# Optimization experiments

Measured on AMD Instinct MI355X. Metric: run time of the kernel, lower is better.

Reference implementation:

```python
import jax, jax.numpy as jnp
import numpy as np

B, T, W, N, D, H, E, NB = 1, 2048, 15, 512, 1024, 150, 20, 10
CP = 2  # coref_prop iterations
NEG = 1e23


def _bucket(d):
    # Lee-et-al style distance bucketing into NB=10 buckets
    d = jnp.clip(d, 0, None)
    logd = (jnp.floor(jnp.log(jnp.maximum(d.astype(jnp.float32), 1.0)) / np.log(2.0)).astype(jnp.int32) + 3)
    return jnp.clip(jnp.where(d <= 4, d, logd), 0, NB - 1)


def _pairs(u, begin, end, Wl, bl, Wr, br, Wp, bp, Edist, Wd, bd, W1, b1, Wo, bo):
    # OptFFpairs: left + right + prod*prod + dist-embedding -> 2-layer FF -> scalar
    l = u @ Wl + bl                                   # [B,N,H]
    r = u @ Wr + br
    s = u @ Wp + bp
    dist = _bucket(begin[:, :, None] - end[:, None, :])  # [B,N,N]
    pe = Edist[dist] @ Wd + bd                        # [B,N,N,H]
    h = l[:, :, None, :] + r[:, None, :, :] + s[:, :, None, :] * s[:, None, :, :] + pe
    h = jax.nn.relu(h)
    h = jax.nn.relu(h @ W1 + b1)
    return (h @ Wo + bo)[..., 0]                      # [B,N,N]


def _add_scores(cs, ss):
    # coref_add_scores: add unary span scores symmetrically, zero the diagonal
    s = cs + ss + jnp.swapaxes(ss, -1, -2)            # ss: [B,N,1]
    eye = jnp.eye(s.shape[-1], dtype=s.dtype)
    return s * (1.0 - eye)


def _overwrite_spans(all_vecs, idx, lengths, values):
    b, t, w, d = all_vecs.shape
    flat = all_vecs.reshape(b, t * w, d)
    k = idx.shape[1]
    mask = (jnp.arange(k)[None, :] < lengths[:, None])[..., None]   # [B,K,1]
    bidx = jnp.arange(b)[:, None]
    orig = flat[bidx, idx]                                          # [B,K,D]
    flat = flat.at[bidx, idx].set(jnp.where(mask, values, orig))
    return flat.reshape(b, t, w, d)


def setup_inputs() -> dict:
    key = jax.random.key(0)
    ks = jax.random.split(key, 24)
    sc = 0.02
    inp = {
        'all_span_vecs': jax.random.normal(ks[0], (B, T, W, D), jnp.float32),
        'span_vecs': jax.random.normal(ks[1], (B, N, D), jnp.float32),
        'span_scores': jax.random.normal(ks[2], (B, N, 1), jnp.float32),
        'triangular_mask': jnp.tril(jnp.ones((N, N), jnp.float32))[None].repeat(B, 0),
        'span_begin': jnp.sort(jax.random.randint(ks[3], (B, N), 0, T), axis=-1).astype(jnp.int32),
        'span_end': jax.random.randint(ks[4], (B, N), 0, T).astype(jnp.int32),
        'prune_indices': jnp.sort(jax.random.permutation(ks[5], T * W)[:N])[None].astype(jnp.int64),
        'span_lengths': jnp.full((B,), N, jnp.int32),
        # OptFFpairs params
        'Wl': jax.random.normal(ks[6], (D, H)) * sc, 'bl': jnp.zeros((H,)),
        'Wr': jax.random.normal(ks[7], (D, H)) * sc, 'br': jnp.zeros((H,)),
        'Wp': jax.random.normal(ks[8], (D, H)) * sc, 'bp': jnp.zeros((H,)),
        'Edist': jax.random.normal(ks[9], (NB, E)) * sc,
        'Wd': jax.random.normal(ks[10], (E, H)) * sc, 'bd': jnp.zeros((H,)),
        'W1': jax.random.normal(ks[11], (H, H)) * sc, 'b1': jnp.zeros((H,)),
        'Wo': jax.random.normal(ks[12], (H, 1)) * sc, 'bo': jnp.zeros((1,)),
        # MyGate params
        'Wg': jax.random.normal(ks[13], (2 * D, D)) * sc, 'bg': jnp.zeros((D,)),
        # coref_pruner params
        'Wpr': jax.random.normal(ks[14], (D, 1)) * sc, 'bpr': jnp.zeros((1,)),
    }
    return inp


def reference(all_span_vecs, span_vecs, span_scores, triangular_mask,
              Wl, bl, Wr, br, Wp, bp, Edist, Wd, bd, W1, b1, Wo, bo,
              Wg, bg, Wpr, bpr,
              span_begin, span_end, prune_indices, span_lengths):
    pargs = (Wl, bl, Wr, br, Wp, bp, Edist, Wd, bd, W1, b1, Wo, bo)
    update = span_vecs
    scores = _pairs(update, span_begin, span_end, *pargs)
    scores = _add_scores(scores, span_scores)
    for _ in range(CP):
        probs = jax.nn.softmax(scores - (1.0 - triangular_mask) * NEG, axis=-1)
        ctxt = jnp.einsum('bij,bjd->bid', probs, update)
        g = jax.nn.sigmoid(jnp.concatenate([update, ctxt], axis=-1) @ Wg + bg)
        update = g * update + (1.0 - g) * ctxt
        scores = _pairs(update, span_begin, span_end, *pargs)
        scores = _add_scores(scores, update @ Wpr + bpr)
    all_out = _overwrite_spans(all_span_vecs, prune_indices, span_lengths, update)
    return (all_out, update, scores)
```

## Files before the change

kernel.cpp:

```cpp
#include <hip/hip_runtime.h>
#include <hip/hip_bf16.h>
#include <cstdint>
#include <cstddef>

typedef __attribute__((ext_vector_type(8))) short short8;
typedef __attribute__((ext_vector_type(4))) float floatx4;

#define MFMA_BF16(a,b,c) __builtin_amdgcn_mfma_f32_16x16x32_bf16((a),(b),(c),0,0,0)

__device__ __forceinline__ float bf2f(short s) {
    return __uint_as_float(((unsigned int)(unsigned short)s) << 16);
}
__device__ __forceinline__ unsigned short f2bf(float f) {
    unsigned int u = __float_as_uint(f);
    u += 0x7FFFu + ((u >> 16) & 1u);
    return (unsigned short)(u >> 16);
}
__device__ __forceinline__ int bucketd(int d) {
    if (d < 0) d = 0;
    if (d <= 4) return d;
    int b = 34 - __clz(d);
    return b > 9 ? 9 : b;
}

__global__ __launch_bounds__(256) void k_prep(
    const float* __restrict__ Wg, const float* __restrict__ Wl, const float* __restrict__ Wr,
    const float* __restrict__ Wp, const float* __restrict__ Wpr,
    const float* __restrict__ span_vecs, const float* __restrict__ span_scores,
    const float* __restrict__ W1g, const float* __restrict__ Edist,
    const float* __restrict__ Wd, const float* __restrict__ bd,
    const float* __restrict__ b1, const float* __restrict__ Wo,
    const float* __restrict__ bl, const float* __restrict__ br, const float* __restrict__ bp,
    const float* __restrict__ bpr,
    unsigned short* __restrict__ WgT, unsigned short* __restrict__ WprojT,
    unsigned short* __restrict__ updT, unsigned short* __restrict__ ubf0,
    float* __restrict__ updatef, float* __restrict__ ss0,
    unsigned short* __restrict__ W1T, unsigned short* __restrict__ Pb,
    float* __restrict__ b1p, float* __restrict__ wop, float* __restrict__ bproj)
{
    __shared__ float tile[32][33];
    int b = blockIdx.x, tid = threadIdx.x;
    if (b < 3040) {
        const float* in; unsigned short* out; int R, C, ldo, rb, cb;
        if (b < 2048)      { in = Wg; out = WgT; R = 2048; C = 1024; ldo = 2048; rb = (b & 63) * 32; cb = (b >> 6) * 32; }
        else if (b < 2208) { int t = b - 2048; in = Wl; out = WprojT;            R = 1024; C = 150; ldo = 1024; rb = (t & 31) * 32; cb = (t >> 5) * 32; }
        else if (b < 2368) { int t = b - 2208; in = Wr; out = WprojT + 192*1024; R = 1024; C = 150; ldo = 1024; rb = (t & 31) * 32; cb = (t >> 5) * 32; }
        else if (b < 2528) { int t = b - 2368; in = Wp; out = WprojT + 384*1024; R = 1024; C = 150; ldo = 1024; rb = (t & 31) * 32; cb = (t >> 5) * 32; }
        else               { int t = b - 2528; in = span_vecs; out = updT;       R = 512;  C = 1024; ldo = 512;  rb = (t & 15) * 32; cb = (t >> 4) * 32; }
        int tx = tid & 31, ty = tid >> 5;
#pragma unroll
        for (int k = 0; k < 4; ++k) {
            int r = rb + ty + k*8, c = cb + tx;
            if (r < R && c < C) tile[ty + k*8][tx] = in[(size_t)r*C + c];
        }
        __syncthreads();
#pragma unroll
        for (int k = 0; k < 4; ++k) {
            int c = cb + ty + k*8, r = rb + tx;
            if (r < R && c < C) out[(size_t)c*ldo + r] = f2bf(tile[tx][ty + k*8]);
        }
        return;
    }
    int g = (b - 3040) * 256 + tid;
    const int gsz = 512 * 256;
    for (int i = g; i < 512*1024; i += gsz) {
        float v = span_vecs[i];
        updatef[i] = v;
        ubf0[(i >> 10)*2048 + (i & 1023)] = f2bf(v);
    }
    for (int i = g; i < 512; i += gsz) ss0[i] = span_scores[i];
    for (int i = g; i < 160*168; i += gsz) {
        int n = i / 168, k = i % 168;
        W1T[i] = f2bf((n < 150 && k < 150) ? W1g[k*150 + n] : 0.f);
    }
    for (int i = g; i < 10*168; i += gsz) {
        int bk = i / 168, h = i % 168;
        float v = 0.f;
        if (h < 150) {
            v = bd[h];
            for (int e = 0; e < 20; ++e) v += Edist[bk*20 + e] * Wd[e*150 + h];
        }
        Pb[i] = f2bf(v);
    }
    for (int i = g; i < 160; i += gsz) {
        b1p[i] = (i < 150) ? b1[i] : 0.f;
        wop[i] = (i < 150) ? Wo[i] : 0.f;
    }
    for (int i = g; i < 640; i += gsz) {
        float v = 0.f;
        if (i < 150) v = bl[i];
        else if (i >= 192 && i < 342) v = br[i - 192];
        else if (i >= 384 && i < 534) v = bp[i - 384];
        else if (i == 576) v = bpr[0];
        bproj[i] = v;
    }
    for (int i = g; i < 42*1024; i += gsz) { WprojT[150*1024 + i] = 0; WprojT[342*1024 + i] = 0; WprojT[534*1024 + i] = 0; }
    for (int i = g; i < 1024; i += gsz) WprojT[576*1024 + i] = f2bf(Wpr[i]);
    for (int i = g; i < 63*1024; i += gsz) WprojT[577*1024 + i] = 0;
}

__global__ __launch_bounds__(256, 4) void k_gemm(
    const unsigned short* __restrict__ A, int lda,
    const unsigned short* __restrict__ BT, int ldb,
    int K, const float* __restrict__ bias,
    float* __restrict__ Cf,
    unsigned short* __restrict__ Cb, int ldcb,
    const float* __restrict__ uf, const float* __restrict__ cf,
    float* __restrict__ uout, unsigned short* __restrict__ updTout,
    float* __restrict__ ss1, int mode)
{
    __shared__ __align__(16) unsigned short As[32*72];
    __shared__ __align__(16) unsigned short Bs[64*72];
    int tid = threadIdx.x;
    int lane = tid & 63, w = tid >> 6;
    int wy = w >> 1, wx = w & 1;
    int ln15 = lane & 15, kg = lane >> 4;
    int m0 = blockIdx.x * 32, n0 = blockIdx.y * 64;
    int rA = tid >> 3, c8 = (tid & 7) * 8;
    const unsigned short* pA  = A  + (size_t)(m0 + rA)*lda + c8;
    const unsigned short* pB0 = BT + (size_t)(n0 + rA)*ldb + c8;
    const unsigned short* pB1 = pB0 + (size_t)32*ldb;
    int nk = K >> 6;
    uint4 ra[2], rb0[2], rb1[2];
    ra[0]  = *(const uint4*)pA;        ra[1]  = *(const uint4*)(pA + 64);
    rb0[0] = *(const uint4*)pB0;       rb0[1] = *(const uint4*)(pB0 + 64);
    rb1[0] = *(const uint4*)pB1;       rb1[1] = *(const uint4*)(pB1 + 64);
    floatx4 acc[2] = {};
    for (int k = 0; k < nk; ++k) {
        int cur = k & 1;
        __syncthreads();
        *(uint4*)(&As[rA*72 + c8])        = ra[cur];
        *(uint4*)(&Bs[rA*72 + c8])        = rb0[cur];
        *(uint4*)(&Bs[(rA + 32)*72 + c8]) = rb1[cur];
        int kn = (k + 2) << 6;
        if (kn < K) {
            ra[cur]  = *(const uint4*)(pA + kn);
            rb0[cur] = *(const uint4*)(pB0 + kn);
            rb1[cur] = *(const uint4*)(pB1 + kn);
        }
        __syncthreads();
#pragma unroll
        for (int ks = 0; ks < 2; ++ks) {
            int ko = ks*32 + kg*8;
            short8 a  = *(const short8*)(&As[(wy*16 + ln15)*72 + ko]);
            short8 b0 = *(const short8*)(&Bs[(wx*32 + ln15)*72 + ko]);
            short8 b1 = *(const short8*)(&Bs[(wx*32 + 16 + ln15)*72 + ko]);
            acc[0] = MFMA_BF16(a, b0, acc[0]);
            acc[1] = MFMA_BF16(a, b1, acc[1]);
        }
    }
#pragma unroll
    for (int nt = 0; nt < 2; ++nt) {
        int n  = n0 + wx*32 + nt*16 + ln15;
        int mb = m0 + wy*16 + kg*4;
        if (mode == 0) {
            float b_ = bias[n];
#pragma unroll
            for (int rg = 0; rg < 4; ++rg) {
                float v = acc[nt][rg] + b_;
                Cb[(size_t)(mb + rg)*ldcb + n] = f2bf(v);
                if (n == 576) ss1[mb + rg] = v;
            }
        } else if (mode == 1) {
#pragma unroll
            for (int rg = 0; rg < 4; ++rg) {
                float v = acc[nt][rg];
                Cf[(size_t)(mb + rg)*1024 + n] = v;
                Cb[(size_t)(mb + rg)*ldcb + n] = f2bf(v);
            }
        } else {
            float b_ = bias[n];
            ushort4 tv; unsigned short* tvp = &tv.x;
#pragma unroll
            for (int rg = 0; rg < 4; ++rg) {
                float v = acc[nt][rg] + b_;
                float gg = 1.f / (1.f + __expf(-v));
                size_t off = (size_t)(mb + rg)*1024 + n;
                float nu = gg*uf[off] + (1.f - gg)*cf[off];
                uout[off] = nu;
                unsigned short nb = f2bf(nu);
                Cb[(size_t)(mb + rg)*ldcb + n] = nb;
                tvp[rg] = nb;
            }
            *(ushort4*)(updTout + (size_t)n*512 + mb) = tv;
        }
    }
}

__global__ __launch_bounds__(256) void k_softmax(const float* __restrict__ scores,
                                                 unsigned short* __restrict__ probsb)
{
    int i = blockIdx.x;
    int tid = threadIdx.x;
    int lane = tid & 63, w = tid >> 6;
    __shared__ float red[8];
    int j0 = tid, j1 = tid + 256;
    bool v0 = (j0 <= i), v1 = (j1 <= i);
    float x0 = v0 ? scores[(size_t)i*512 + j0] : -1e30f;
    float x1 = v1 ? scores[(size_t)i*512 + j1] : -1e30f;
    float mx = fmaxf(x0, x1);
    for (int off = 32; off; off >>= 1) mx = fmaxf(mx, __shfl_xor(mx, off));
    if (lane == 0) red[w] = mx;
    __syncthreads();
    mx = fmaxf(fmaxf(red[0], red[1]), fmaxf(red[2], red[3]));
    float p0 = v0 ? __expf(x0 - mx) : 0.f;
    float p1 = v1 ? __expf(x1 - mx) : 0.f;
    float sm = p0 + p1;
    for (int off = 32; off; off >>= 1) sm += __shfl_xor(sm, off);
    if (lane == 0) red[4 + w] = sm;
    __syncthreads();
    float inv = 1.f / (red[4] + red[5] + red[6] + red[7]);
    probsb[(size_t)i*512 + j0] = f2bf(p0 * inv);
    probsb[(size_t)i*512 + j1] = f2bf(p1 * inv);
}

__global__ __launch_bounds__(512, 2) void k_pair(
    const unsigned short* __restrict__ lrsb,
    const unsigned short* __restrict__ Pb,
    const unsigned short* __restrict__ W1Tg,
    const float* __restrict__ b1p, const float* __restrict__ wop,
    const float* __restrict__ bo,
    const float* __restrict__ ssbuf,
    const int* __restrict__ beginp, const int* __restrict__ endp,
    float* __restrict__ scoresOut)
{
    __shared__ __align__(16) unsigned short smR[74*168];
    __shared__ __align__(16) unsigned short smB[2][160*36];
    int tid = threadIdx.x;
    int i0 = blockIdx.x * 16, j0 = blockIdx.y * 16;
    for (int c = tid; c < 74*21; c += 512) {
        int row = c / 21, c8 = (c % 21) * 8;
        const unsigned short* src;
        if (row < 16)      src = lrsb + (size_t)(i0 + row)*640 + c8;
        else if (row < 32) src = lrsb + (size_t)(i0 + row - 16)*640 + 384 + c8;
        else if (row < 48) src = lrsb + (size_t)(j0 + row - 32)*640 + 192 + c8;
        else if (row < 64) src = lrsb + (size_t)(j0 + row - 48)*640 + 384 + c8;
        else               src = Pb + (size_t)(row - 64)*168 + c8;
        *(uint4*)(&smR[row*168 + c8]) = *(const uint4*)src;
    }
    int lane = tid & 63, w = tid >> 6;
    int ln15 = lane & 15, kg = lane >> 4;
    int iw = i0 + 2*w;
    int ej = endp[j0 + ln15];
    int da = bucketd(beginp[iw] - ej);
    int db = bucketd(beginp[iw + 1] - ej);
    int rW = tid >> 2, cW = (tid & 3) * 8;
    int rW2 = 128 + rW;
    bool has2 = (tid < 128);
    uint4 w0 = *(const uint4*)(W1Tg + (size_t)rW*168 + cW);
    uint4 w1 = has2 ? *(const uint4*)(W1Tg + (size_t)rW2*168 + cW) : make_uint4(0,0,0,0);
    floatx4 acc[2][10] = {};
    for (int kb = 0; kb < 5; ++kb) {
        int cur = kb & 1;
        *(uint4*)(&smB[cur][rW*36 + cW]) = w0;
        if (has2) *(uint4*)(&smB[cur][rW2*36 + cW]) = w1;
        if (kb < 4) {
            int kf = (kb + 1)*32;
            w0 = *(const uint4*)(W1Tg + (size_t)rW*168 + kf + cW);
            if (has2) w1 = *(const uint4*)(W1Tg + (size_t)rW2*168 + kf + cW);
        }
        __syncthreads();
        int ko = kb*32 + kg*8;
        short8 rv  = *(const short8*)(&smR[(32 + ln15)*168 + ko]);
        short8 sjv = *(const short8*)(&smR[(48 + ln15)*168 + ko]);
        short8 hf[2];
#pragma unroll
        for (int mt = 0; mt < 2; ++mt) {
            int ri = 2*w + mt;
            short8 lv  = *(const short8*)(&smR[ri*168 + ko]);
            short8 siv = *(const short8*)(&smR[(16 + ri)*168 + ko]);
            int d = mt ? db : da;
            short8 pv  = *(const short8*)(&smR[(64 + d)*168 + ko]);
#pragma unroll
            for (int t = 0; t < 8; ++t) {
                float h = bf2f(lv[t]) + bf2f(rv[t]) + bf2f(siv[t]) * bf2f(sjv[t]) + bf2f(pv[t]);
                h = fmaxf(h, 0.f);
                hf[mt][t] = (short)f2bf(h);
            }
        }
#pragma unroll
        for (int nt = 0; nt < 10; ++nt) {
            short8 bv = *(const short8*)(&smB[cur][(nt*16 + ln15)*36 + kg*8]);
            acc[0][nt] = MFMA_BF16(hf[0], bv, acc[0][nt]);
            acc[1][nt] = MFMA_BF16(hf[1], bv, acc[1][nt]);
        }
    }
    float part[2][4] = {};
#pragma unroll
    for (int nt = 0; nt < 10; ++nt) {
        int n = nt*16 + ln15;
        float b1v = b1p[n], wv = wop[n];
#pragma unroll
        for (int mt = 0; mt < 2; ++mt)
#pragma unroll
            for (int rg = 0; rg < 4; ++rg)
                part[mt][rg] += fmaxf(acc[mt][nt][rg] + b1v, 0.f) * wv;
    }
    float bo0 = bo[0];
#pragma unroll
    for (int mt = 0; mt < 2; ++mt) {
#pragma unroll
        for (int rg = 0; rg < 4; ++rg) {
            float p = part[mt][rg];
            p += __shfl_xor(p, 1); p += __shfl_xor(p, 2);
            p += __shfl_xor(p, 4); p += __shfl_xor(p, 8);
            part[mt][rg] = p;
        }
        if (ln15 == 0) {
            int i = iw + mt;
            float ssi = ssbuf[i];
            int jb = j0 + kg*4;
            float r0 = part[mt][0] + bo0 + ssi + ssbuf[jb + 0]; if (i == jb + 0) r0 = 0.f;
            float r1 = part[mt][1] + bo0 + ssi + ssbuf[jb + 1]; if (i == jb + 1) r1 = 0.f;
            float r2 = part[mt][2] + bo0 + ssi + ssbuf[jb + 2]; if (i == jb + 2) r2 = 0.f;
            float r3 = part[mt][3] + bo0 + ssi + ssbuf[jb + 3]; if (i == jb + 3) r3 = 0.f;
            float4 vv; vv.x = r0; vv.y = r1; vv.z = r2; vv.w = r3;
            *(float4*)(scoresOut + (size_t)i*512 + jb) = vv;
        }
    }
}

__global__ __launch_bounds__(256) void k_final(const float* __restrict__ allv,
                                               const int* __restrict__ prune,
                                               const int* __restrict__ lengths,
                                               const float* __restrict__ updatef,
                                               float* __restrict__ out)
{
    int row = blockIdx.x;
    if (row < 30720) {
        int len = lengths[0];
        if (len > 512) len = 512;
        int lo = 0, hi = len;
        while (lo < hi) { int mid = (lo + hi) >> 1; if (prune[mid] < row) lo = mid + 1; else hi = mid; }
        bool found = (lo < len) && (prune[lo] == row);
        const float4* src = found ? (const float4*)(updatef + (size_t)lo*1024)
                                  : (const float4*)(allv + (size_t)row*1024);
        ((float4*)(out + (size_t)row*1024))[threadIdx.x] = src[threadIdx.x];
    } else {
        int k = row - 30720;
        ((float4*)(out + (size_t)row*1024))[threadIdx.x] =
            ((const float4*)(updatef + (size_t)k*1024))[threadIdx.x];
    }
}

extern "C" void kernel_launch(void* const* d_in, const int* in_sizes, int n_in,
                              void* d_out, int out_size, void* d_ws, size_t ws_size,
                              hipStream_t stream) {
    const float* all_span    = (const float*)d_in[0];
    const float* span_vecs   = (const float*)d_in[1];
    const float* span_scores = (const float*)d_in[2];
    const int*   beginp      = (const int*)d_in[4];
    const int*   endp        = (const int*)d_in[5];
    const int*   prune       = (const int*)d_in[6];
    const int*   lengths     = (const int*)d_in[7];
    const float* Wl = (const float*)d_in[8];  const float* bl = (const float*)d_in[9];
    const float* Wr = (const float*)d_in[10]; const float* br = (const float*)d_in[11];
    const float* Wp = (const float*)d_in[12]; const float* bp = (const float*)d_in[13];
    const float* Edist = (const float*)d_in[14];
    const float* Wd = (const float*)d_in[15]; const float* bd = (const float*)d_in[16];
    const float* W1 = (const float*)d_in[17]; const float* b1 = (const float*)d_in[18];
    const float* Wo = (const float*)d_in[19]; const float* bo = (const float*)d_in[20];
    const float* Wg = (const float*)d_in[21]; const float* bg = (const float*)d_in[22];
    const float* Wpr = (const float*)d_in[23]; const float* bpr = (const float*)d_in[24];

    char* wsb = (char*)d_ws;
    size_t o = 0;
    auto nxt = [&](size_t b) { size_t r = o; o += (b + 255) & ~(size_t)255; return r; };
    float* updatef  = (float*)(wsb + nxt(512*1024*4));
    float* ctxtf    = (float*)(wsb + nxt(512*1024*4));
    float* scoresws = (float*)(wsb + nxt(512*512*4));
    float* ss0      = (float*)(wsb + nxt(512*4));
    float* ss1      = (float*)(wsb + nxt(512*4));
    float* bproj    = (float*)(wsb + nxt(640*4));
    float* b1p      = (float*)(wsb + nxt(160*4));
    float* wop      = (float*)(wsb + nxt(160*4));
    unsigned short* ubf0    = (unsigned short*)(wsb + nxt(512*2048*2));
    unsigned short* ubf1    = (unsigned short*)(wsb + nxt(512*2048*2));
    unsigned short* updT    = (unsigned short*)(wsb + nxt(1024*512*2));
    unsigned short* probsb  = (unsigned short*)(wsb + nxt(512*512*2));
    unsigned short* lrsb    = (unsigned short*)(wsb + nxt(512*640*2));
    unsigned short* WgT     = (unsigned short*)(wsb + nxt(1024*2048*2));
    unsigned short* WprojT  = (unsigned short*)(wsb + nxt(640*1024*2));
    unsigned short* W1T     = (unsigned short*)(wsb + nxt(160*168*2));
    unsigned short* Pb      = (unsigned short*)(wsb + nxt(10*168*2));

    float* outp = (float*)d_out;
    float* out_scores = outp + 31457280 + 524288;

    k_prep<<<3552, 256, 0, stream>>>(Wg, Wl, Wr, Wp, Wpr, span_vecs, span_scores,
                                     W1, Edist, Wd, bd, b1, Wo, bl, br, bp, bpr,
                                     WgT, WprojT, updT, ubf0, updatef, ss0,
                                     W1T, Pb, b1p, wop, bproj);

    k_gemm<<<dim3(16, 10), 256, 0, stream>>>(ubf0, 2048, WprojT, 1024, 1024, bproj,
                                             nullptr, lrsb, 640,
                                             nullptr, nullptr, nullptr, nullptr, ss1, 0);
    k_pair<<<dim3(32, 32), 512, 0, stream>>>(lrsb, Pb, W1T, b1p, wop, bo, ss0, beginp, endp, scoresws);

    unsigned short* ucur = ubf0;
    unsigned short* unxt = ubf1;
    for (int it = 0; it < 2; ++it) {
        k_softmax<<<512, 256, 0, stream>>>(scoresws, probsb);
        k_gemm<<<dim3(16, 16), 256, 0, stream>>>(probsb, 512, updT, 512, 512, nullptr,
                                                 ctxtf, ucur + 1024, 2048,
                                                 nullptr, nullptr, nullptr, nullptr, nullptr, 1);
        k_gemm<<<dim3(16, 16), 256, 0, stream>>>(ucur, 2048, WgT, 2048, 2048, bg,
                                                 nullptr, unxt, 2048,
                                                 updatef, ctxtf, updatef, updT, nullptr, 2);
        k_gemm<<<dim3(16, 10), 256, 0, stream>>>(unxt, 2048, WprojT, 1024, 1024, bproj,
                                                 nullptr, lrsb, 640,
                                                 nullptr, nullptr, nullptr, nullptr, ss1, 0);
        float* sdst = (it == 1) ? out_scores : scoresws;
        k_pair<<<dim3(32, 32), 512, 0, stream>>>(lrsb, Pb, W1T, b1p, wop, bo, ss1, beginp, endp, sdst);
        unsigned short* t = ucur; ucur = unxt; unxt = t;
    }

    k_final<<<31232, 256, 0, stream>>>(all_span, prune, lengths, updatef, outp);
}
```

Baseline: 536.6 us.

## Fuse all stages into one persistent kernel with software grid barriers

Replaces the sequence of prep, GEMM, pair, softmax and final-copy launches with a single persistent kernel of 256 blocks of 512 threads. A counter-based global barrier separates the phases, and each phase loops over its tiles or rows by block index. The GEMM tile grows to 64x64 so the 8 waves per block are used. This removes per-launch overhead and idle gaps between launches. In exchange, the memory-bound prep and final-copy phases run at low occupancy, many blocks sit idle in the small GEMM phases, and each barrier adds spin-wait latency.

```diff
diff --git a/kernel.cpp b/kernel.cpp
--- a/kernel.cpp
+++ b/kernel.cpp
@@ -7,6 +7,7 @@
 typedef __attribute__((ext_vector_type(4))) float floatx4;
 
 #define MFMA_BF16(a,b,c) __builtin_amdgcn_mfma_f32_16x16x32_bf16((a),(b),(c),0,0,0)
+#define NBLK 256
 
 __device__ __forceinline__ float bf2f(short s) {
     return __uint_as_float(((unsigned int)(unsigned short)s) << 16);
@@ -23,7 +24,23 @@
     return b > 9 ? 9 : b;
 }
 
-__global__ __launch_bounds__(256) void k_prep(
+__device__ __forceinline__ void gbar(unsigned* cnt, int idx) {
+    __syncthreads();
+    if (threadIdx.x == 0) {
+        __threadfence();
+        __hip_atomic_fetch_add(&cnt[idx], 1u, __ATOMIC_RELAXED, __HIP_MEMORY_SCOPE_AGENT);
+        while (__hip_atomic_load(&cnt[idx], __ATOMIC_RELAXED, __HIP_MEMORY_SCOPE_AGENT) < (unsigned)NBLK)
+            __builtin_amdgcn_s_sleep(8);
+        __threadfence();
+    }
+    __syncthreads();
+}
+
+__global__ void k_zero(unsigned* __restrict__ cnt) {
+    if (threadIdx.x < 64) cnt[threadIdx.x] = 0;
+}
+
+__device__ void prep_phase(char* smc, int tid,
     const float* __restrict__ Wg, const float* __restrict__ Wl, const float* __restrict__ Wr,
     const float* __restrict__ Wp, const float* __restrict__ Wpr,
     const float* __restrict__ span_vecs, const float* __restrict__ span_scores,
@@ -38,31 +55,40 @@
     unsigned short* __restrict__ W1T, unsigned short* __restrict__ Pb,
     float* __restrict__ b1p, float* __restrict__ wop, float* __restrict__ bproj)
 {
-    __shared__ float tile[32][33];
-    int b = blockIdx.x, tid = threadIdx.x;
-    if (b < 3040) {
-        const float* in; unsigned short* out; int R, C, ldo, rb, cb;
-        if (b < 2048)      { in = Wg; out = WgT; R = 2048; C = 1024; ldo = 2048; rb = (b & 63) * 32; cb = (b >> 6) * 32; }
-        else if (b < 2208) { int t = b - 2048; in = Wl; out = WprojT;            R = 1024; C = 150; ldo = 1024; rb = (t & 31) * 32; cb = (t >> 5) * 32; }
-        else if (b < 2368) { int t = b - 2208; in = Wr; out = WprojT + 192*1024; R = 1024; C = 150; ldo = 1024; rb = (t & 31) * 32; cb = (t >> 5) * 32; }
-        else if (b < 2528) { int t = b - 2368; in = Wp; out = WprojT + 384*1024; R = 1024; C = 150; ldo = 1024; rb = (t & 31) * 32; cb = (t >> 5) * 32; }
-        else               { int t = b - 2528; in = span_vecs; out = updT;       R = 512;  C = 1024; ldo = 512;  rb = (t & 15) * 32; cb = (t >> 4) * 32; }
-        int tx = tid & 31, ty = tid >> 5;
-#pragma unroll
-        for (int k = 0; k < 4; ++k) {
-            int r = rb + ty + k*8, c = cb + tx;
-            if (r < R && c < C) tile[ty + k*8][tx] = in[(size_t)r*C + c];
-        }
-        __syncthreads();
-#pragma unroll
-        for (int k = 0; k < 4; ++k) {
-            int c = cb + ty + k*8, r = rb + tx;
-            if (r < R && c < C) out[(size_t)c*ldo + r] = f2bf(tile[tx][ty + k*8]);
-        }
-        return;
-    }
-    int g = (b - 3040) * 256 + tid;
-    const int gsz = 512 * 256;
+    float (*tp)[32][33] = (float (*)[32][33])smc;
+    int half = tid >> 8, t256 = tid & 255;
+    int tx = t256 & 31, ty = t256 >> 5;
+    for (int it = 0; it < 6; ++it) {
+        int t = it*512 + blockIdx.x*2 + half;
+        const float* in = nullptr; unsigned short* out = nullptr;
+        int R = 0, C = 0, ldo = 0, rb = 0, cb = 0;
+        bool act = (t < 3040);
+        if (act) {
+            if (t < 2048)      { in = Wg; out = WgT; R = 2048; C = 1024; ldo = 2048; rb = (t & 63)*32; cb = (t >> 6)*32; }
+            else if (t < 2208) { int q = t - 2048; in = Wl; out = WprojT;            R = 1024; C = 150; ldo = 1024; rb = (q & 31)*32; cb = (q >> 5)*32; }
+            else if (t < 2368) { int q = t - 2208; in = Wr; out = WprojT + 192*1024; R = 1024; C = 150; ldo = 1024; rb = (q & 31)*32; cb = (q >> 5)*32; }
+            else if (t < 2528) { int q = t - 2368; in = Wp; out = WprojT + 384*1024; R = 1024; C = 150; ldo = 1024; rb = (q & 31)*32; cb = (q >> 5)*32; }
+            else               { int q = t - 2528; in = span_vecs; out = updT;       R = 512;  C = 1024; ldo = 512;  rb = (q & 15)*32; cb = (q >> 4)*32; }
+        }
+        if (act) {
+#pragma unroll
+            for (int k = 0; k < 4; ++k) {
+                int r = rb + ty + k*8, c = cb + tx;
+                if (r < R && c < C) tp[half][ty + k*8][tx] = in[(size_t)r*C + c];
+            }
+        }
+        __syncthreads();
+        if (act) {
+#pragma unroll
+            for (int k = 0; k < 4; ++k) {
+                int c = cb + ty + k*8, r = rb + tx;
+                if (r < R && c < C) out[(size_t)c*ldo + r] = f2bf(tp[half][tx][ty + k*8]);
+            }
+        }
+        __syncthreads();
+    }
+    int g = blockIdx.x*512 + tid;
+    const int gsz = NBLK*512;
     for (int i = g; i < 512*1024; i += gsz) {
         float v = span_vecs[i];
         updatef[i] = v;
@@ -99,44 +125,40 @@
     for (int i = g; i < 63*1024; i += gsz) WprojT[577*1024 + i] = 0;
 }
 
-__global__ __launch_bounds__(256, 4) void k_gemm(
+__device__ void gemm_phase(char* smc, int tid,
     const unsigned short* __restrict__ A, int lda,
     const unsigned short* __restrict__ BT, int ldb,
-    int K, const float* __restrict__ bias,
-    float* __restrict__ Cf,
-    unsigned short* __restrict__ Cb, int ldcb,
+    int K, int mtiles, int ntiles, const float* __restrict__ bias,
+    float* __restrict__ Cf, unsigned short* __restrict__ Cb, int ldcb,
     const float* __restrict__ uf, const float* __restrict__ cf,
     float* __restrict__ uout, unsigned short* __restrict__ updTout,
     float* __restrict__ ss1, int mode)
 {
-    __shared__ __align__(16) unsigned short As[32*72];
-    __shared__ __align__(16) unsigned short Bs[64*72];
-    int tid = threadIdx.x;
+    int b = blockIdx.x;
+    if (b >= mtiles*ntiles) return;
+    unsigned short* As = (unsigned short*)smc;
+    unsigned short* Bs = (unsigned short*)(smc + 64*72*2);
+    int m0 = (b % mtiles)*64, n0 = (b / mtiles)*64;
     int lane = tid & 63, w = tid >> 6;
     int wy = w >> 1, wx = w & 1;
     int ln15 = lane & 15, kg = lane >> 4;
-    int m0 = blockIdx.x * 32, n0 = blockIdx.y * 64;
-    int rA = tid >> 3, c8 = (tid & 7) * 8;
-    const unsigned short* pA  = A  + (size_t)(m0 + rA)*lda + c8;
-    const unsigned short* pB0 = BT + (size_t)(n0 + rA)*ldb + c8;
-    const unsigned short* pB1 = pB0 + (size_t)32*ldb;
+    int rA = tid >> 3, c8 = (tid & 7)*8;
+    const unsigned short* pA = A  + (size_t)(m0 + rA)*lda + c8;
+    const unsigned short* pB = BT + (size_t)(n0 + rA)*ldb + c8;
+    uint4 ra[2], rb[2];
+    ra[0] = *(const uint4*)pA;        rb[0] = *(const uint4*)pB;
+    ra[1] = *(const uint4*)(pA + 64); rb[1] = *(const uint4*)(pB + 64);
+    floatx4 acc[2] = {};
     int nk = K >> 6;
-    uint4 ra[2], rb0[2], rb1[2];
-    ra[0]  = *(const uint4*)pA;        ra[1]  = *(const uint4*)(pA + 64);
-    rb0[0] = *(const uint4*)pB0;       rb0[1] = *(const uint4*)(pB0 + 64);
-    rb1[0] = *(const uint4*)pB1;       rb1[1] = *(const uint4*)(pB1 + 64);
-    floatx4 acc[2] = {};
     for (int k = 0; k < nk; ++k) {
         int cur = k & 1;
         __syncthreads();
-        *(uint4*)(&As[rA*72 + c8])        = ra[cur];
-        *(uint4*)(&Bs[rA*72 + c8])        = rb0[cur];
-        *(uint4*)(&Bs[(rA + 32)*72 + c8]) = rb1[cur];
+        *(uint4*)(&As[rA*72 + c8]) = ra[cur];
+        *(uint4*)(&Bs[rA*72 + c8]) = rb[cur];
         int kn = (k + 2) << 6;
         if (kn < K) {
-            ra[cur]  = *(const uint4*)(pA + kn);
-            rb0[cur] = *(const uint4*)(pB0 + kn);
-            rb1[cur] = *(const uint4*)(pB1 + kn);
+            ra[cur] = *(const uint4*)(pA + kn);
+            rb[cur] = *(const uint4*)(pB + kn);
         }
         __syncthreads();
 #pragma unroll
@@ -187,160 +209,212 @@
     }
 }
 
-__global__ __launch_bounds__(256) void k_softmax(const float* __restrict__ scores,
-                                                 unsigned short* __restrict__ probsb)
-{
-    int i = blockIdx.x;
-    int tid = threadIdx.x;
+__device__ void softmax_phase(char* smc, int tid,
+    const float* __restrict__ scores, unsigned short* __restrict__ probsb)
+{
+    float* red = (float*)smc;
     int lane = tid & 63, w = tid >> 6;
-    __shared__ float red[8];
-    int j0 = tid, j1 = tid + 256;
-    bool v0 = (j0 <= i), v1 = (j1 <= i);
-    float x0 = v0 ? scores[(size_t)i*512 + j0] : -1e30f;
-    float x1 = v1 ? scores[(size_t)i*512 + j1] : -1e30f;
-    float mx = fmaxf(x0, x1);
-    for (int off = 32; off; off >>= 1) mx = fmaxf(mx, __shfl_xor(mx, off));
-    if (lane == 0) red[w] = mx;
-    __syncthreads();
-    mx = fmaxf(fmaxf(red[0], red[1]), fmaxf(red[2], red[3]));
-    float p0 = v0 ? __expf(x0 - mx) : 0.f;
-    float p1 = v1 ? __expf(x1 - mx) : 0.f;
-    float sm = p0 + p1;
-    for (int off = 32; off; off >>= 1) sm += __shfl_xor(sm, off);
-    if (lane == 0) red[4 + w] = sm;
-    __syncthreads();
-    float inv = 1.f / (red[4] + red[5] + red[6] + red[7]);
-    probsb[(size_t)i*512 + j0] = f2bf(p0 * inv);
-    probsb[(size_t)i*512 + j1] = f2bf(p1 * inv);
-}
-
-__global__ __launch_bounds__(512, 2) void k_pair(
-    const unsigned short* __restrict__ lrsb,
-    const unsigned short* __restrict__ Pb,
+    for (int r = blockIdx.x; r < 512; r += NBLK) {
+        bool v = (tid <= r);
+        float x = v ? scores[(size_t)r*512 + tid] : -1e30f;
+        float mx = x;
+        for (int off = 32; off; off >>= 1) mx = fmaxf(mx, __shfl_xor(mx, off));
+        if (lane == 0) red[w] = mx;
+        __syncthreads();
+        mx = red[0];
+#pragma unroll
+        for (int q = 1; q < 8; ++q) mx = fmaxf(mx, red[q]);
+        float p = v ? __expf(x - mx) : 0.f;
+        float s = p;
+        for (int off = 32; off; off >>= 1) s += __shfl_xor(s, off);
+        __syncthreads();
+        if (lane == 0) red[w] = s;
+        __syncthreads();
+        float tot = red[0];
+#pragma unroll
+        for (int q = 1; q < 8; ++q) tot += red[q];
+        probsb[(size_t)r*512 + tid] = f2bf(p / tot);
+        __syncthreads();
+    }
+}
+
+__device__ void pair_phase(char* smc, int tid,
+    const unsigned short* __restrict__ lrsb, const unsigned short* __restrict__ Pb,
     const unsigned short* __restrict__ W1Tg,
-    const float* __restrict__ b1p, const float* __restrict__ wop,
-    const float* __restrict__ bo,
+    const float* __restrict__ b1p, const float* __restrict__ wop, const float* __restrict__ bo,
     const float* __restrict__ ssbuf,
     const int* __restrict__ beginp, const int* __restrict__ endp,
     float* __restrict__ scoresOut)
 {
-    __shared__ __align__(16) unsigned short smR[74*168];
-    __shared__ __align__(16) unsigned short smB[2][160*36];
-    int tid = threadIdx.x;
-    int i0 = blockIdx.x * 16, j0 = blockIdx.y * 16;
-    for (int c = tid; c < 74*21; c += 512) {
-        int row = c / 21, c8 = (c % 21) * 8;
-        const unsigned short* src;
-        if (row < 16)      src = lrsb + (size_t)(i0 + row)*640 + c8;
-        else if (row < 32) src = lrsb + (size_t)(i0 + row - 16)*640 + 384 + c8;
-        else if (row < 48) src = lrsb + (size_t)(j0 + row - 32)*640 + 192 + c8;
-        else if (row < 64) src = lrsb + (size_t)(j0 + row - 48)*640 + 384 + c8;
-        else               src = Pb + (size_t)(row - 64)*168 + c8;
-        *(uint4*)(&smR[row*168 + c8]) = *(const uint4*)src;
-    }
+    unsigned short* smR = (unsigned short*)smc;
+    unsigned short* smB = (unsigned short*)(smc + 74*168*2);
     int lane = tid & 63, w = tid >> 6;
     int ln15 = lane & 15, kg = lane >> 4;
-    int iw = i0 + 2*w;
-    int ej = endp[j0 + ln15];
-    int da = bucketd(beginp[iw] - ej);
-    int db = bucketd(beginp[iw + 1] - ej);
-    int rW = tid >> 2, cW = (tid & 3) * 8;
-    int rW2 = 128 + rW;
-    bool has2 = (tid < 128);
-    uint4 w0 = *(const uint4*)(W1Tg + (size_t)rW*168 + cW);
-    uint4 w1 = has2 ? *(const uint4*)(W1Tg + (size_t)rW2*168 + cW) : make_uint4(0,0,0,0);
-    floatx4 acc[2][10] = {};
-    for (int kb = 0; kb < 5; ++kb) {
-        int cur = kb & 1;
-        *(uint4*)(&smB[cur][rW*36 + cW]) = w0;
-        if (has2) *(uint4*)(&smB[cur][rW2*36 + cW]) = w1;
-        if (kb < 4) {
-            int kf = (kb + 1)*32;
-            w0 = *(const uint4*)(W1Tg + (size_t)rW*168 + kf + cW);
-            if (has2) w1 = *(const uint4*)(W1Tg + (size_t)rW2*168 + kf + cW);
-        }
-        __syncthreads();
-        int ko = kb*32 + kg*8;
-        short8 rv  = *(const short8*)(&smR[(32 + ln15)*168 + ko]);
-        short8 sjv = *(const short8*)(&smR[(48 + ln15)*168 + ko]);
-        short8 hf[2];
+    int rW = tid >> 2, cW = (tid & 3)*8;
+    int rW2 = 128 + rW; bool has2 = (tid < 128);
+    float bo0 = bo[0];
+    for (int t = blockIdx.x; t < 1024; t += NBLK) {
+        int i0 = (t & 31)*16, j0 = (t >> 5)*16;
+        __syncthreads();
+        for (int c = tid; c < 74*21; c += 512) {
+            int row = c / 21, c8 = (c % 21)*8;
+            const unsigned short* src;
+            if (row < 16)      src = lrsb + (size_t)(i0 + row)*640 + c8;
+            else if (row < 32) src = lrsb + (size_t)(i0 + row - 16)*640 + 384 + c8;
+            else if (row < 48) src = lrsb + (size_t)(j0 + row - 32)*640 + 192 + c8;
+            else if (row < 64) src = lrsb + (size_t)(j0 + row - 48)*640 + 384 + c8;
+            else               src = Pb + (size_t)(row - 64)*168 + c8;
+            *(uint4*)(&smR[row*168 + c8]) = *(const uint4*)src;
+        }
+        int iw = i0 + 2*w;
+        int ej = endp[j0 + ln15];
+        int da = bucketd(beginp[iw] - ej);
+        int db = bucketd(beginp[iw + 1] - ej);
+        uint4 w0 = *(const uint4*)(W1Tg + (size_t)rW*168 + cW);
+        uint4 w1 = has2 ? *(const uint4*)(W1Tg + (size_t)rW2*168 + cW) : make_uint4(0,0,0,0);
+        floatx4 acc[2][10] = {};
+        for (int kb = 0; kb < 5; ++kb) {
+            int cur = kb & 1;
+            *(uint4*)(&smB[cur*5760 + rW*36 + cW]) = w0;
+            if (has2) *(uint4*)(&smB[cur*5760 + rW2*36 + cW]) = w1;
+            if (kb < 4) {
+                int kf = (kb + 1)*32;
+                w0 = *(const uint4*)(W1Tg + (size_t)rW*168 + kf + cW);
+                if (has2) w1 = *(const uint4*)(W1Tg + (size_t)rW2*168 + kf + cW);
+            }
+            __syncthreads();
+            int ko = kb*32 + kg*8;
+            short8 rv  = *(const short8*)(&smR[(32 + ln15)*168 + ko]);
+            short8 sjv = *(const short8*)(&smR[(48 + ln15)*168 + ko]);
+            short8 hf[2];
+#pragma unroll
+            for (int mt = 0; mt < 2; ++mt) {
+                int ri = 2*w + mt;
+                short8 lv  = *(const short8*)(&smR[ri*168 + ko]);
+                short8 siv = *(const short8*)(&smR[(16 + ri)*168 + ko]);
+                int d = mt ? db : da;
+                short8 pv  = *(const short8*)(&smR[(64 + d)*168 + ko]);
+#pragma unroll
+                for (int u = 0; u < 8; ++u) {
+                    float h = bf2f(lv[u]) + bf2f(rv[u]) + bf2f(siv[u])*bf2f(sjv[u]) + bf2f(pv[u]);
+                    h = fmaxf(h, 0.f);
+                    hf[mt][u] = (short)f2bf(h);
+                }
+            }
+#pragma unroll
+            for (int nt = 0; nt < 10; ++nt) {
+                short8 bv = *(const short8*)(&smB[cur*5760 + (nt*16 + ln15)*36 + kg*8]);
+                acc[0][nt] = MFMA_BF16(hf[0], bv, acc[0][nt]);
+                acc[1][nt] = MFMA_BF16(hf[1], bv, acc[1][nt]);
+            }
+        }
+        float part[2][4] = {};
+#pragma unroll
+        for (int nt = 0; nt < 10; ++nt) {
+            int n = nt*16 + ln15;
+            float b1v = b1p[n], wv = wop[n];
+#pragma unroll
+            for (int mt = 0; mt < 2; ++mt)
+#pragma unroll
+                for (int rg = 0; rg < 4; ++rg)
+                    part[mt][rg] += fmaxf(acc[mt][nt][rg] + b1v, 0.f)*wv;
+        }
 #pragma unroll
         for (int mt = 0; mt < 2; ++mt) {
-            int ri = 2*w + mt;
-            short8 lv  = *(const short8*)(&smR[ri*168 + ko]);
-            short8 siv = *(const short8*)(&smR[(16 + ri)*168 + ko]);
-            int d = mt ? db : da;
-            short8 pv  = *(const short8*)(&smR[(64 + d)*168 + ko]);
-#pragma unroll
-            for (int t = 0; t < 8; ++t) {
-                float h = bf2f(lv[t]) + bf2f(rv[t]) + bf2f(siv[t]) * bf2f(sjv[t]) + bf2f(pv[t]);
-                h = fmaxf(h, 0.f);
-                hf[mt][t] = (short)f2bf(h);
-            }
-        }
-#pragma unroll
-        for (int nt = 0; nt < 10; ++nt) {
-            short8 bv = *(const short8*)(&smB[cur][(nt*16 + ln15)*36 + kg*8]);
-            acc[0][nt] = MFMA_BF16(hf[0], bv, acc[0][nt]);
-            acc[1][nt] = MFMA_BF16(hf[1], bv, acc[1][nt]);
-        }
-    }
-    float part[2][4] = {};
-#pragma unroll
-    for (int nt = 0; nt < 10; ++nt) {
-        int n = nt*16 + ln15;
-        float b1v = b1p[n], wv = wop[n];
-#pragma unroll
-        for (int mt = 0; mt < 2; ++mt)
-#pragma unroll
-            for (int rg = 0; rg < 4; ++rg)
-                part[mt][rg] += fmaxf(acc[mt][nt][rg] + b1v, 0.f) * wv;
-    }
-    float bo0 = bo[0];
-#pragma unroll
-    for (int mt = 0; mt < 2; ++mt) {
-#pragma unroll
-        for (int rg = 0; rg < 4; ++rg) {
-            float p = part[mt][rg];
-            p += __shfl_xor(p, 1); p += __shfl_xor(p, 2);
-            p += __shfl_xor(p, 4); p += __shfl_xor(p, 8);
-            part[mt][rg] = p;
-        }
-        if (ln15 == 0) {
-            int i = iw + mt;
-            float ssi = ssbuf[i];
-            int jb = j0 + kg*4;
-            float r0 = part[mt][0] + bo0 + ssi + ssbuf[jb + 0]; if (i == jb + 0) r0 = 0.f;
-            float r1 = part[mt][1] + bo0 + ssi + ssbuf[jb + 1]; if (i == jb + 1) r1 = 0.f;
-            float r2 = part[mt][2] + bo0 + ssi + ssbuf[jb + 2]; if (i == jb + 2) r2 = 0.f;
-            float r3 = part[mt][3] + bo0 + ssi + ssbuf[jb + 3]; if (i == jb + 3) r3 = 0.f;
-            float4 vv; vv.x = r0; vv.y = r1; vv.z = r2; vv.w = r3;
-            *(float4*)(scoresOut + (size_t)i*512 + jb) = vv;
-        }
-    }
-}
-
-__global__ __launch_bounds__(256) void k_final(const float* __restrict__ allv,
-                                               const int* __restrict__ prune,
-                                               const int* __restrict__ lengths,
-                                               const float* __restrict__ updatef,
-                                               float* __restrict__ out)
-{
-    int row = blockIdx.x;
-    if (row < 30720) {
-        int len = lengths[0];
-        if (len > 512) len = 512;
-        int lo = 0, hi = len;
-        while (lo < hi) { int mid = (lo + hi) >> 1; if (prune[mid] < row) lo = mid + 1; else hi = mid; }
-        bool found = (lo < len) && (prune[lo] == row);
-        const float4* src = found ? (const float4*)(updatef + (size_t)lo*1024)
-                                  : (const float4*)(allv + (size_t)row*1024);
-        ((float4*)(out + (size_t)row*1024))[threadIdx.x] = src[threadIdx.x];
-    } else {
-        int k = row - 30720;
-        ((float4*)(out + (size_t)row*1024))[threadIdx.x] =
-            ((const float4*)(updatef + (size_t)k*1024))[threadIdx.x];
-    }
+#pragma unroll
+            for (int rg = 0; rg < 4; ++rg) {
+                float p = part[mt][rg];
+                p += __shfl_xor(p, 1); p += __shfl_xor(p, 2);
+                p += __shfl_xor(p, 4); p += __shfl_xor(p, 8);
+                part[mt][rg] = p;
+            }
+            if (ln15 == 0) {
+                int i = iw + mt;
+                float ssi = ssbuf[i];
+                int jb = j0 + kg*4;
+                float r0 = part[mt][0] + bo0 + ssi + ssbuf[jb + 0]; if (i == jb + 0) r0 = 0.f;
+                float r1 = part[mt][1] + bo0 + ssi + ssbuf[jb + 1]; if (i == jb + 1) r1 = 0.f;
+                float r2 = part[mt][2] + bo0 + ssi + ssbuf[jb + 2]; if (i == jb + 2) r2 = 0.f;
+                float r3 = part[mt][3] + bo0 + ssi + ssbuf[jb + 3]; if (i == jb + 3) r3 = 0.f;
+                float4 vv; vv.x = r0; vv.y = r1; vv.z = r2; vv.w = r3;
+                *(float4*)(scoresOut + (size_t)i*512 + jb) = vv;
+            }
+        }
+    }
+}
+
+__device__ void final_phase(int tid,
+    const float* __restrict__ allv, const int* __restrict__ prune,
+    const int* __restrict__ lengths, const float* __restrict__ updatef,
+    float* __restrict__ out)
+{
+    int half = tid >> 8, t256 = tid & 255;
+    int len = lengths[0]; if (len > 512) len = 512;
+    for (int rr = blockIdx.x*2 + half; rr < 31232; rr += 512) {
+        const float4* src;
+        if (rr < 30720) {
+            int lo = 0, hi = len;
+            while (lo < hi) { int mid = (lo + hi) >> 1; if (prune[mid] < rr) lo = mid + 1; else hi = mid; }
+            bool found = (lo < len) && (prune[lo] == rr);
+            src = found ? (const float4*)(updatef + (size_t)lo*1024)
+                        : (const float4*)(allv + (size_t)rr*1024);
+        } else {
+            src = (const float4*)(updatef + (size_t)(rr - 30720)*1024);
+        }
+        ((float4*)(out + (size_t)rr*1024))[t256] = src[t256];
+    }
+}
+
+__global__ __launch_bounds__(512, 2) void k_mega(
+    const float* all_span, const float* span_vecs, const float* span_scores,
+    const int* beginp, const int* endp, const int* prune, const int* lengths,
+    const float* Wl, const float* bl, const float* Wr, const float* br,
+    const float* Wp, const float* bp, const float* Edist, const float* Wd, const float* bd,
+    const float* W1, const float* b1, const float* Wo, const float* bo,
+    const float* Wg, const float* bg, const float* Wpr, const float* bpr,
+    float* updatef, float* ctxtf, float* scoresws, float* ss0, float* ss1,
+    float* bproj, float* b1p, float* wop,
+    unsigned short* ubf0, unsigned short* ubf1, unsigned short* updT,
+    unsigned short* probsb, unsigned short* lrsb, unsigned short* WgT,
+    unsigned short* WprojT, unsigned short* W1T, unsigned short* Pb,
+    unsigned* cnt, float* out)
+{
+    __shared__ __align__(16) char smc[49152];
+    int tid = threadIdx.x;
+    float* out_scores = out + 31457280 + 524288;
+    int bi = 0;
+
+    prep_phase(smc, tid, Wg, Wl, Wr, Wp, Wpr, span_vecs, span_scores,
+               W1, Edist, Wd, bd, b1, Wo, bl, br, bp, bpr,
+               WgT, WprojT, updT, ubf0, updatef, ss0, W1T, Pb, b1p, wop, bproj);
+    gbar(cnt, bi++);
+
+    gemm_phase(smc, tid, ubf0, 2048, WprojT, 1024, 1024, 8, 10, bproj,
+               nullptr, lrsb, 640, nullptr, nullptr, nullptr, nullptr, ss1, 0);
+    gbar(cnt, bi++);
+    pair_phase(smc, tid, lrsb, Pb, W1T, b1p, wop, bo, ss0, beginp, endp, scoresws);
+    gbar(cnt, bi++);
+
+    unsigned short* ucur = ubf0;
+    unsigned short* unxt = ubf1;
+    for (int it = 0; it < 2; ++it) {
+        softmax_phase(smc, tid, scoresws, probsb);
+        gbar(cnt, bi++);
+        gemm_phase(smc, tid, probsb, 512, updT, 512, 512, 8, 16, nullptr,
+                   ctxtf, ucur + 1024, 2048, nullptr, nullptr, nullptr, nullptr, nullptr, 1);
+        gbar(cnt, bi++);
+        gemm_phase(smc, tid, ucur, 2048, WgT, 2048, 2048, 8, 16, bg,
+                   nullptr, unxt, 2048, updatef, ctxtf, updatef, updT, nullptr, 2);
+        gbar(cnt, bi++);
+        gemm_phase(smc, tid, unxt, 2048, WprojT, 1024, 1024, 8, 10, bproj,
+                   nullptr, lrsb, 640, nullptr, nullptr, nullptr, nullptr, ss1, 0);
+        gbar(cnt, bi++);
+        float* sdst = (it == 1) ? out_scores : scoresws;
+        pair_phase(smc, tid, lrsb, Pb, W1T, b1p, wop, bo, ss1, beginp, endp, sdst);
+        if (it == 0) gbar(cnt, bi++);
+        unsigned short* t = ucur; ucur = unxt; unxt = t;
+    }
+    final_phase(tid, all_span, prune, lengths, updatef, out);
 }
 
 extern "C" void kernel_launch(void* const* d_in, const int* in_sizes, int n_in,
@@ -383,37 +457,13 @@
     unsigned short* WprojT  = (unsigned short*)(wsb + nxt(640*1024*2));
     unsigned short* W1T     = (unsigned short*)(wsb + nxt(160*168*2));
     unsigned short* Pb      = (unsigned short*)(wsb + nxt(10*168*2));
-
-    float* outp = (float*)d_out;
-    float* out_scores = outp + 31457280 + 524288;
-
-    k_prep<<<3552, 256, 0, stream>>>(Wg, Wl, Wr, Wp, Wpr, span_vecs, span_scores,
-                                     W1, Edist, Wd, bd, b1, Wo, bl, br, bp, bpr,
-                                     WgT, WprojT, updT, ubf0, updatef, ss0,
-                                     W1T, Pb, b1p, wop, bproj);
-
-    k_gemm<<<dim3(16, 10), 256, 0, stream>>>(ubf0, 2048, WprojT, 1024, 1024, bproj,
-                                             nullptr, lrsb, 640,
-                                             nullptr, nullptr, nullptr, nullptr, ss1, 0);
-    k_pair<<<dim3(32, 32), 512, 0, stream>>>(lrsb, Pb, W1T, b1p, wop, bo, ss0, beginp, endp, scoresws);
-
-    unsigned short* ucur = ubf0;
-    unsigned short* unxt = ubf1;
-    for (int it = 0; it < 2; ++it) {
-        k_softmax<<<512, 256, 0, stream>>>(scoresws, probsb);
-        k_gemm<<<dim3(16, 16), 256, 0, stream>>>(probsb, 512, updT, 512, 512, nullptr,
-                                                 ctxtf, ucur + 1024, 2048,
-                                                 nullptr, nullptr, nullptr, nullptr, nullptr, 1);
-        k_gemm<<<dim3(16, 16), 256, 0, stream>>>(ucur, 2048, WgT, 2048, 2048, bg,
-                                                 nullptr, unxt, 2048,
-                                                 updatef, ctxtf, updatef, updT, nullptr, 2);
-        k_gemm<<<dim3(16, 10), 256, 0, stream>>>(unxt, 2048, WprojT, 1024, 1024, bproj,
-                                                 nullptr, lrsb, 640,
-                                                 nullptr, nullptr, nullptr, nullptr, ss1, 0);
-        float* sdst = (it == 1) ? out_scores : scoresws;
-        k_pair<<<dim3(32, 32), 512, 0, stream>>>(lrsb, Pb, W1T, b1p, wop, bo, ss1, beginp, endp, sdst);
-        unsigned short* t = ucur; ucur = unxt; unxt = t;
-    }
-
-    k_final<<<31232, 256, 0, stream>>>(all_span, prune, lengths, updatef, outp);
-}
+    unsigned*       cnt     = (unsigned*)(wsb + nxt(64*4));
+
+    k_zero<<<1, 64, 0, stream>>>(cnt);
+    k_mega<<<NBLK, 512, 0, stream>>>(all_span, span_vecs, span_scores,
+        beginp, endp, prune, lengths,
+        Wl, bl, Wr, br, Wp, bp, Edist, Wd, bd, W1, b1, Wo, bo, Wg, bg, Wpr, bpr,
+        updatef, ctxtf, scoresws, ss0, ss1, bproj, b1p, wop,
+        ubf0, ubf1, updT, probsb, lrsb, WgT, WprojT, W1T, Pb,
+        cnt, (float*)d_out);
+}
```

New measurement: 1.129 ms. 2.1x slower.
